# Performance work log

Measured on AMD Instinct MI355X. Metric: run time of the kernel, lower is better.

## Reference

```python
import jax, jax.numpy as jnp
import numpy as np

VOCAB = 2          # len(CHAR_VOCAB) in source
CE = 16            # char_embed_dim
CNN_OUT = 32 + 64 + 128  # 224
EMBED = 64


def _conv1d(x, w, b, pad):
    # x: [N, Cin, L]; w: [Cout, Cin, K]; torch Conv1d semantics
    y = jax.lax.conv_general_dilated(
        x, w, window_strides=(1,), padding=[(pad, pad)],
        dimension_numbers=('NCH', 'OIH', 'NCH'))
    return y + b[None, :, None]


def setup_inputs() -> dict:
    key = jax.random.key(0)
    ks = jax.random.split(key, 12)
    B, S, MC = 32, 2048, 20
    char_ids = jax.random.randint(ks[0], (B, S, MC), 0, VOCAB, dtype=jnp.int64)
    E = jax.random.normal(ks[1], (VOCAB, CE), jnp.float32)
    E = E.at[0].set(0.0)  # padding_idx=0
    s = 0.05
    return {
        'char_ids': char_ids,
        'E': E,
        'W1': jax.random.normal(ks[2], (32, CE, 1), jnp.float32) * s,
        'b1': jnp.zeros((32,), jnp.float32),
        'W2': jax.random.normal(ks[3], (64, CE, 2), jnp.float32) * s,
        'b2': jnp.zeros((64,), jnp.float32),
        'W3': jax.random.normal(ks[4], (128, CE, 3), jnp.float32) * s,
        'b3': jnp.zeros((128,), jnp.float32),
        'Ht_W': jax.random.normal(ks[5], (CNN_OUT, CNN_OUT), jnp.float32) * s,
        'Ht_b': jnp.zeros((CNN_OUT,), jnp.float32),
        'Hg_W': jax.random.normal(ks[6], (CNN_OUT, CNN_OUT), jnp.float32) * s,
        'Hg_b': jnp.zeros((CNN_OUT,), jnp.float32),
        'P_W': jax.random.normal(ks[7], (EMBED, CNN_OUT), jnp.float32) * s,
        'P_b': jnp.zeros((EMBED,), jnp.float32),
    }


def reference(char_ids, E, W1, b1, W2, b2, W3, b3, Ht_W, Ht_b, Hg_W, Hg_b, P_W, P_b):
    B, S, MC = char_ids.shape
    ids = char_ids.reshape(-1, MC)                      # [N, MC]
    emb = E[ids]                                        # [N, MC, CE]
    x = jnp.transpose(emb, (0, 2, 1))                   # [N, CE, MC]
    p1 = jnp.max(jax.nn.relu(_conv1d(x, W1, b1, 0)), axis=2)  # [N, 32]
    p2 = jnp.max(jax.nn.relu(_conv1d(x, W2, b2, 1)), axis=2)  # [N, 64]
    p3 = jnp.max(jax.nn.relu(_conv1d(x, W3, b3, 1)), axis=2)  # [N, 128]
    cnn = jnp.concatenate([p1, p2, p3], axis=1)         # [N, 224]
    t = jax.nn.relu(cnn @ Ht_W.T + Ht_b)
    g = jax.nn.sigmoid(cnn @ Hg_W.T + Hg_b)
    hw = g * t + (1.0 - g) * cnn
    out = hw @ P_W.T + P_b                              # [N, 64]
    return out.reshape(B, S, -1)
```

## Files before the change

kernel.cpp:

```cpp
#include <hip/hip_runtime.h>


typedef _Float16 f16;
typedef __attribute__((ext_vector_type(8))) _Float16 f16x8;
typedef __attribute__((ext_vector_type(4))) float f32x4;

#define LC1   0
#define LRAW2 96
#define LT2   672
#define LRAW3 1696
#define LT3LO 5152
#define LT3HI 7200
#define WOFFB    18944
#define PBASE    100352
#define NWTH     114688
#define TKEY_OFF 278528
#define UOUT_OFF 544768
#define NKEYS    4096
#define WSPLIT_BLOCKS 448
#define LUT_BLOCKS 4
#define CROW 232

__device__ __forceinline__ f16x8 hmax8(f16x8 a, f16x8 b) {
  return __builtin_elementwise_max(a, b);
}

__device__ __forceinline__ f16x8 pin8(f16x8 v) {
  union { f16x8 v; unsigned w[4]; } x; x.v = v;
  asm volatile("" : "+v"(x.w[0]), "+v"(x.w[1]), "+v"(x.w[2]), "+v"(x.w[3]) :: "memory");
  return x.v;
}

__global__ __launch_bounds__(256) void prep_key_kernel(
    const float* __restrict__ E,
    const float* __restrict__ W1, const float* __restrict__ b1,
    const float* __restrict__ W2, const float* __restrict__ b2,
    const float* __restrict__ W3, const float* __restrict__ b3,
    const float* __restrict__ HtW, const float* __restrict__ HgW,
    const float* __restrict__ PW, const int* __restrict__ ids,
    f16* __restrict__ tab, f16* __restrict__ wsb,
    unsigned* __restrict__ tokkey, int n_tok)
{
  const int tid = threadIdx.x;
  if (blockIdx.x >= WSPLIT_BLOCKS + LUT_BLOCKS) {
    int t = (blockIdx.x - WSPLIT_BLOCKS - LUT_BLOCKS) * 256 + tid;
    if (t >= n_tok) return;
    const int4* idp4 = (const int4*)(ids + (size_t)t * 20);
    int st[21];
#pragma unroll
    for (int q = 0; q < 5; q++) {
      int4 v = idp4[q];
      st[q * 4 + 1] = v.x; st[q * 4 + 2] = v.y;
      st[q * 4 + 3] = v.z; st[q * 4 + 4] = v.w;
    }
    unsigned m3i = 0;
#pragma unroll
    for (int l = 1; l <= 18; l++)
      m3i |= 1u << ((st[l] << 2) | (st[l + 1] << 1) | st[l + 2]);
    tokkey[t] = m3i | ((unsigned)st[1] << 8) | ((unsigned)st[2] << 9)
              | ((unsigned)st[19] << 10) | ((unsigned)st[20] << 11);
    return;
  }
  if (blockIdx.x < WSPLIT_BLOCKS) {
    int idx = blockIdx.x * 256 + tid;
    if (idx < NWTH) {
      int e, isG = 0, isP = 0;
      if (idx < 50176)        { e = idx; }
      else if (idx < 100352)  { e = idx - 50176; isG = 1; }
      else                    { e = idx - 100352; isP = 1; }
      int col = e / 224, k = e - col * 224;
      int nf = col >> 4, kf = k >> 5, kr = k & 31;
      int lane = (col & 15) + ((kr >> 3) << 4), j = kr & 7;
      if (!isP) {
        int off = nf * 7168 + (isG * 7 + kf) * 512 + lane * 8 + j;
        wsb[off] = (f16)(isG ? HgW[e] : HtW[e]);
      } else {
        float w = PW[e];
        f16 hi = (f16)w;
        int off = PBASE + nf * 7168 + kf * 512 + lane * 8 + j;
        wsb[off] = hi;
        wsb[off + 3584] = (f16)(w - (float)hi);
      }
    }
    return;
  }

  __shared__ float X[3][16];
  __shared__ float U1[3][32];
  __shared__ float U2[9][64];
  __shared__ float U3[27][128];
  const int gid = (blockIdx.x - WSPLIT_BLOCKS) * 256 + tid;
  const int gsz = LUT_BLOCKS * 256;
  if (tid < 48) { int s = tid >> 4, i = tid & 15; X[s][i] = (s == 0) ? 0.f : E[(s - 1) * 16 + i]; }
  __syncthreads();

  for (int idx = tid; idx < 96; idx += 256) {
    int s = idx >> 5, c = idx & 31;
    float acc = b1[c];
#pragma unroll
    for (int i = 0; i < 16; i++) acc += W1[c * 16 + i] * X[s][i];
    U1[s][c] = acc;
  }
  for (int idx = tid; idx < 576; idx += 256) {
    int p = idx >> 6, c = idx & 63;
    int sa = p / 3, sb = p % 3;
    float acc = b2[c];
#pragma unroll
    for (int i = 0; i < 16; i++)
      acc += W2[c * 32 + i * 2 + 0] * X[sa][i] + W2[c * 32 + i * 2 + 1] * X[sb][i];
    U2[p][c] = acc;
  }
  for (int idx = tid; idx < 3456; idx += 256) {
    int p = idx >> 7, c = idx & 127;
    int sa = p / 9, sb = (p / 3) % 3, sc = p % 3;
    float acc = b3[c];
#pragma unroll
    for (int i = 0; i < 16; i++)
      acc += W3[c * 48 + i * 3 + 0] * X[sa][i]
           + W3[c * 48 + i * 3 + 1] * X[sb][i]
           + W3[c * 48 + i * 3 + 2] * X[sc][i];
    U3[p][c] = acc;
  }
  __syncthreads();

  for (int idx = gid; idx < 96; idx += gsz) {
    int r = idx >> 5, c = idx & 31;
    float v = (r == 0) ? fmaxf(U1[1][c], U1[2][c]) : U1[r][c];
    tab[LC1 + idx] = (f16)v;
  }
  for (int idx = gid; idx < 576; idx += gsz) tab[LRAW2 + idx] = (f16)U2[idx >> 6][idx & 63];
  for (int idx = gid; idx < 3456; idx += gsz) tab[LRAW3 + idx] = (f16)U3[idx >> 7][idx & 127];
  for (int idx = gid; idx < 1024; idx += gsz) {
    int s = idx >> 6, c = idx & 63;
    float m = -65504.f;
#pragma unroll
    for (int b = 0; b < 4; b++)
      if ((s >> b) & 1) m = fmaxf(m, U2[4 + 3 * (b >> 1) + (b & 1)][c]);
    tab[LT2 + idx] = (f16)m;
  }
  for (int idx = gid; idx < 2048; idx += gsz) {
    int s = idx >> 7, c = idx & 127;
    float m = -65504.f;
#pragma unroll
    for (int b = 0; b < 4; b++)
      if ((s >> b) & 1) m = fmaxf(m, U3[13 + 3 * (b >> 1) + (b & 1)][c]);
    tab[LT3LO + idx] = (f16)m;
    m = -65504.f;
#pragma unroll
    for (int b = 0; b < 4; b++)
      if ((s >> b) & 1) m = fmaxf(m, U3[22 + 3 * (b >> 1) + (b & 1)][c]);
    tab[LT3HI + idx] = (f16)m;
  }
}

__global__ __launch_bounds__(256) void ucompute_kernel(
    const f16* __restrict__ tab, const f16* __restrict__ wsb,
    const float* __restrict__ Htb, const float* __restrict__ Hgb,
    const float* __restrict__ Pb, float* __restrict__ uout)
{
  __shared__ __attribute__((aligned(16))) f16 cnn[16 * CROW];

  const int tid = threadIdx.x;
  const int wave = tid >> 6, lane = tid & 63;
  const int kbase = blockIdx.x * 16;
  const int lrow = lane & 15;
  const int kg8 = (lane >> 4) * 8;
  const int rr0 = (lane >> 4) * 4;

  const int p1row = tid >> 4;
  const int p1g = tid & 15;
  unsigned mw, mb;
  {
    unsigned key = (unsigned)(kbase + p1row);
    unsigned m3i = key & 255u;
    int st1 = 1 + (int)((key >> 8) & 1),  st2 = 1 + (int)((key >> 9) & 1);
    int st19 = 1 + (int)((key >> 10) & 1), st20 = 1 + (int)((key >> 11) & 1);
    unsigned m2i = 0, mchar = 0;
#pragma unroll
    for (int p = 0; p < 8; p++)
      if ((m3i >> p) & 1) {
        m2i |= (1u << (p >> 1)) | (1u << (p & 3));
        mchar |= (1u << ((p >> 2) & 1)) | (1u << ((p >> 1) & 1)) | (1u << (p & 1));
      }
    unsigned sel = (mchar == 3u) ? 0u : ((mchar & 1u) ? 1u : 2u);
    mw = m3i | (m2i << 8) | (sel << 12);
    mb = (unsigned)st1 | ((unsigned)(st20 * 3) << 4)
       | ((unsigned)(st1 * 3 + st2) << 8) | ((unsigned)(st19 * 9 + st20 * 3) << 16);
  }

  const f16x8 KZ = {0, 0, 0, 0, 0, 0, 0, 0};
  {
    const int m3 = mw & 255;
    f16x8 v = hmax8(*(const f16x8*)(tab + LT3LO + (m3 & 15) * 128 + p1g * 8),
                    *(const f16x8*)(tab + LT3HI + ((m3 >> 4) & 15) * 128 + p1g * 8));
    v = hmax8(v, *(const f16x8*)(tab + LRAW3 + ((mb >> 8) & 15) * 128 + p1g * 8));
    v = hmax8(v, *(const f16x8*)(tab + LRAW3 + ((mb >> 16) & 31) * 128 + p1g * 8));
    *(f16x8*)&cnn[p1row * CROW + 96 + p1g * 8] = hmax8(v, KZ);
    if (p1g < 8) {
      f16x8 u = *(const f16x8*)(tab + LT2 + ((mw >> 8) & 15) * 64 + p1g * 8);
      u = hmax8(u, *(const f16x8*)(tab + LRAW2 + (mb & 15) * 64 + p1g * 8));
      u = hmax8(u, *(const f16x8*)(tab + LRAW2 + ((mb >> 4) & 15) * 64 + p1g * 8));
      *(f16x8*)&cnn[p1row * CROW + 32 + p1g * 8] = hmax8(u, KZ);
    }
    if (p1g < 4) {
      int sel = (mw >> 12) & 3;
      f16x8 w = *(const f16x8*)(tab + LC1 + sel * 32 + p1g * 8);
      *(f16x8*)&cnn[p1row * CROW + p1g * 8] = hmax8(w, KZ);
    }
  }
  __syncthreads();

  f16x8 af[7];
#pragma unroll
  for (int kf = 0; kf < 7; kf++)
    af[kf] = *(const f16x8*)&cnn[lrow * CROW + kf * 32 + kg8];
#pragma unroll
  for (int kf = 0; kf < 7; kf++) af[kf] = pin8(af[kf]);
  __syncthreads();

  const f16* wbase = wsb + lane * 8;
  const int nf_cnt = (wave < 2) ? 4 : 3;
  for (int i = 0; i < nf_cnt; i++) {
    const int nf = wave + i * 4;
    const int col = nf * 16 + lrow;
    const f16* p_ = wbase + nf * 7168;
    const float bt = Htb[col], bg = Hgb[col];
    f32x4 aT = {bt, bt, bt, bt};
    f32x4 aG = {bg, bg, bg, bg};
#pragma unroll
    for (int kf = 0; kf < 7; kf++) {
      f16x8 wTv = *(const f16x8*)(p_ + kf * 512);
      f16x8 wGv = *(const f16x8*)(p_ + 3584 + kf * 512);
      aT = __builtin_amdgcn_mfma_f32_16x16x32_f16(af[kf], wTv, aT, 0, 0, 0);
      aG = __builtin_amdgcn_mfma_f32_16x16x32_f16(af[kf], wGv, aG, 0, 0, 0);
    }
#pragma unroll
    for (int r = 0; r < 4; r++) {
      int row = rr0 + r;
      float t  = fmaxf(aT[r], 0.f);
      float gg = __builtin_amdgcn_rcpf(1.f + __expf(-aG[r]));
      float cv = (float)cnn[row * CROW + col];
      cnn[row * CROW + col] = (f16)(cv + gg * (t - cv));
    }
  }
  __syncthreads();

  f16x8 ah[7];
#pragma unroll
  for (int kf = 0; kf < 7; kf++)
    ah[kf] = *(const f16x8*)&cnn[lrow * CROW + kf * 32 + kg8];
  {
    const int col = wave * 16 + lrow;
    const float bp = Pb[col];
    f32x4 ac = {bp, bp, bp, bp};
    const f16* ph = wbase + PBASE + wave * 7168;
#pragma unroll
    for (int kf = 0; kf < 7; kf++) {
      f16x8 wh = *(const f16x8*)(ph + kf * 512);
      f16x8 wl = *(const f16x8*)(ph + 3584 + kf * 512);
      ac = __builtin_amdgcn_mfma_f32_16x16x32_f16(ah[kf], wh, ac, 0, 0, 0);
      ac = __builtin_amdgcn_mfma_f32_16x16x32_f16(ah[kf], wl, ac, 0, 0, 0);
    }
#pragma unroll
    for (int r = 0; r < 4; r++)
      uout[(size_t)(kbase + rr0 + r) * 64 + col] = ac[r];
  }
}

__global__ __launch_bounds__(256) void scatter_kernel(
    const unsigned* __restrict__ tokkey, const float* __restrict__ uout,
    float* __restrict__ out, int n_tok)
{
  int gid = blockIdx.x * 256 + threadIdx.x;
  int t = gid >> 2, q = gid & 3;
  if (t >= n_tok) return;
  unsigned s = tokkey[t];
  const float4* src = (const float4*)(uout + (size_t)s * 64 + q * 16);
  float4* dst = (float4*)(out + (size_t)t * 64 + q * 16);
  dst[0] = src[0]; dst[1] = src[1]; dst[2] = src[2]; dst[3] = src[3];
}

extern "C" void kernel_launch(void* const* d_in, const int* in_sizes, int n_in,
                              void* d_out, int out_size, void* d_ws, size_t ws_size,
                              hipStream_t stream) {
  const int*   ids = (const int*)d_in[0];
  const float* E   = (const float*)d_in[1];
  const float* W1  = (const float*)d_in[2];
  const float* b1  = (const float*)d_in[3];
  const float* W2  = (const float*)d_in[4];
  const float* b2  = (const float*)d_in[5];
  const float* W3  = (const float*)d_in[6];
  const float* b3  = (const float*)d_in[7];
  const float* HtW = (const float*)d_in[8];
  const float* Htb = (const float*)d_in[9];
  const float* HgW = (const float*)d_in[10];
  const float* Hgb = (const float*)d_in[11];
  const float* PW  = (const float*)d_in[12];
  const float* Pb  = (const float*)d_in[13];
  float* out = (float*)d_out;
  char* ws = (char*)d_ws;
  f16* tab = (f16*)ws;
  f16* wsb = (f16*)(ws + WOFFB);
  unsigned* tokkey = (unsigned*)(ws + TKEY_OFF);
  float* uout = (float*)(ws + UOUT_OFF);

  const int n_tok = in_sizes[0] / 20;
  const int key_blocks = (n_tok + 255) / 256;

  prep_key_kernel<<<WSPLIT_BLOCKS + LUT_BLOCKS + key_blocks, 256, 0, stream>>>(
      E, W1, b1, W2, b2, W3, b3, HtW, HgW, PW, ids, tab, wsb, tokkey, n_tok);
  ucompute_kernel<<<NKEYS / 16, 256, 0, stream>>>(tab, wsb, Htb, Hgb, Pb, uout);
  scatter_kernel<<<((size_t)n_tok * 4 + 255) / 256, 256, 0, stream>>>(
      tokkey, uout, out, n_tok);
}
```

Baseline: 31.90 us.

## Fuse LUT build and weight conversion into ucompute, merge key computation into scatter

Drops the separate prep kernel. Each ucompute block now rebuilds the conv lookup tables in shared memory and converts the fp32 highway and projection weights to fp16 on the fly from global memory, instead of reading a pre-swizzled fp16 buffer. The per-token key computation moves into the scatter kernel, so the tokkey round-trip through global memory goes away. This cuts one launch and the intermediate buffers, but every one of the 256 blocks redundantly computes the small conv tables, and weight loads become uncoalesced strided fp32 reads plus conversions.

```diff
diff --git a/kernel.cpp b/kernel.cpp
--- a/kernel.cpp
+++ b/kernel.cpp
@@ -11,15 +11,10 @@
 #define LRAW3 1696
 #define LT3LO 5152
 #define LT3HI 7200
-#define WOFFB    18944
-#define PBASE    100352
-#define NWTH     114688
-#define TKEY_OFF 278528
-#define UOUT_OFF 544768
-#define NKEYS    4096
-#define WSPLIT_BLOCKS 448
-#define LUT_BLOCKS 4
-#define CROW 232
+#define TABSZ 9248
+#define NKEYS 4096
+#define CROW  232
+#define UOUT_OFF 0
 
 __device__ __forceinline__ f16x8 hmax8(f16x8 a, f16x8 b) {
   return __builtin_elementwise_max(a, b);
@@ -31,133 +26,43 @@
   return x.v;
 }
 
-__global__ __launch_bounds__(256) void prep_key_kernel(
+__device__ __forceinline__ f16x8 ldcvt(const float* __restrict__ p) {
+  float4 a = *(const float4*)p;
+  float4 b = *(const float4*)(p + 4);
+  f16x8 r;
+  r[0] = (f16)a.x; r[1] = (f16)a.y; r[2] = (f16)a.z; r[3] = (f16)a.w;
+  r[4] = (f16)b.x; r[5] = (f16)b.y; r[6] = (f16)b.z; r[7] = (f16)b.w;
+  return r;
+}
+
+__device__ __forceinline__ void ldcvt2(const float* __restrict__ p,
+                                       f16x8& hi, f16x8& lo) {
+  float4 a = *(const float4*)p;
+  float4 b = *(const float4*)(p + 4);
+  float wv[8] = {a.x, a.y, a.z, a.w, b.x, b.y, b.z, b.w};
+#pragma unroll
+  for (int j = 0; j < 8; j++) {
+    f16 h = (f16)wv[j];
+    hi[j] = h;
+    lo[j] = (f16)(wv[j] - (float)h);
+  }
+}
+
+__global__ __launch_bounds__(256) void fused_ucompute(
     const float* __restrict__ E,
     const float* __restrict__ W1, const float* __restrict__ b1,
     const float* __restrict__ W2, const float* __restrict__ b2,
     const float* __restrict__ W3, const float* __restrict__ b3,
     const float* __restrict__ HtW, const float* __restrict__ HgW,
-    const float* __restrict__ PW, const int* __restrict__ ids,
-    f16* __restrict__ tab, f16* __restrict__ wsb,
-    unsigned* __restrict__ tokkey, int n_tok)
+    const float* __restrict__ PW,
+    const float* __restrict__ Htb, const float* __restrict__ Hgb,
+    const float* __restrict__ Pb, float* __restrict__ uout)
 {
-  const int tid = threadIdx.x;
-  if (blockIdx.x >= WSPLIT_BLOCKS + LUT_BLOCKS) {
-    int t = (blockIdx.x - WSPLIT_BLOCKS - LUT_BLOCKS) * 256 + tid;
-    if (t >= n_tok) return;
-    const int4* idp4 = (const int4*)(ids + (size_t)t * 20);
-    int st[21];
-#pragma unroll
-    for (int q = 0; q < 5; q++) {
-      int4 v = idp4[q];
-      st[q * 4 + 1] = v.x; st[q * 4 + 2] = v.y;
-      st[q * 4 + 3] = v.z; st[q * 4 + 4] = v.w;
-    }
-    unsigned m3i = 0;
-#pragma unroll
-    for (int l = 1; l <= 18; l++)
-      m3i |= 1u << ((st[l] << 2) | (st[l + 1] << 1) | st[l + 2]);
-    tokkey[t] = m3i | ((unsigned)st[1] << 8) | ((unsigned)st[2] << 9)
-              | ((unsigned)st[19] << 10) | ((unsigned)st[20] << 11);
-    return;
-  }
-  if (blockIdx.x < WSPLIT_BLOCKS) {
-    int idx = blockIdx.x * 256 + tid;
-    if (idx < NWTH) {
-      int e, isG = 0, isP = 0;
-      if (idx < 50176)        { e = idx; }
-      else if (idx < 100352)  { e = idx - 50176; isG = 1; }
-      else                    { e = idx - 100352; isP = 1; }
-      int col = e / 224, k = e - col * 224;
-      int nf = col >> 4, kf = k >> 5, kr = k & 31;
-      int lane = (col & 15) + ((kr >> 3) << 4), j = kr & 7;
-      if (!isP) {
-        int off = nf * 7168 + (isG * 7 + kf) * 512 + lane * 8 + j;
-        wsb[off] = (f16)(isG ? HgW[e] : HtW[e]);
-      } else {
-        float w = PW[e];
-        f16 hi = (f16)w;
-        int off = PBASE + nf * 7168 + kf * 512 + lane * 8 + j;
-        wsb[off] = hi;
-        wsb[off + 3584] = (f16)(w - (float)hi);
-      }
-    }
-    return;
-  }
-
   __shared__ float X[3][16];
   __shared__ float U1[3][32];
   __shared__ float U2[9][64];
   __shared__ float U3[27][128];
-  const int gid = (blockIdx.x - WSPLIT_BLOCKS) * 256 + tid;
-  const int gsz = LUT_BLOCKS * 256;
-  if (tid < 48) { int s = tid >> 4, i = tid & 15; X[s][i] = (s == 0) ? 0.f : E[(s - 1) * 16 + i]; }
-  __syncthreads();
-
-  for (int idx = tid; idx < 96; idx += 256) {
-    int s = idx >> 5, c = idx & 31;
-    float acc = b1[c];
-#pragma unroll
-    for (int i = 0; i < 16; i++) acc += W1[c * 16 + i] * X[s][i];
-    U1[s][c] = acc;
-  }
-  for (int idx = tid; idx < 576; idx += 256) {
-    int p = idx >> 6, c = idx & 63;
-    int sa = p / 3, sb = p % 3;
-    float acc = b2[c];
-#pragma unroll
-    for (int i = 0; i < 16; i++)
-      acc += W2[c * 32 + i * 2 + 0] * X[sa][i] + W2[c * 32 + i * 2 + 1] * X[sb][i];
-    U2[p][c] = acc;
-  }
-  for (int idx = tid; idx < 3456; idx += 256) {
-    int p = idx >> 7, c = idx & 127;
-    int sa = p / 9, sb = (p / 3) % 3, sc = p % 3;
-    float acc = b3[c];
-#pragma unroll
-    for (int i = 0; i < 16; i++)
-      acc += W3[c * 48 + i * 3 + 0] * X[sa][i]
-           + W3[c * 48 + i * 3 + 1] * X[sb][i]
-           + W3[c * 48 + i * 3 + 2] * X[sc][i];
-    U3[p][c] = acc;
-  }
-  __syncthreads();
-
-  for (int idx = gid; idx < 96; idx += gsz) {
-    int r = idx >> 5, c = idx & 31;
-    float v = (r == 0) ? fmaxf(U1[1][c], U1[2][c]) : U1[r][c];
-    tab[LC1 + idx] = (f16)v;
-  }
-  for (int idx = gid; idx < 576; idx += gsz) tab[LRAW2 + idx] = (f16)U2[idx >> 6][idx & 63];
-  for (int idx = gid; idx < 3456; idx += gsz) tab[LRAW3 + idx] = (f16)U3[idx >> 7][idx & 127];
-  for (int idx = gid; idx < 1024; idx += gsz) {
-    int s = idx >> 6, c = idx & 63;
-    float m = -65504.f;
-#pragma unroll
-    for (int b = 0; b < 4; b++)
-      if ((s >> b) & 1) m = fmaxf(m, U2[4 + 3 * (b >> 1) + (b & 1)][c]);
-    tab[LT2 + idx] = (f16)m;
-  }
-  for (int idx = gid; idx < 2048; idx += gsz) {
-    int s = idx >> 7, c = idx & 127;
-    float m = -65504.f;
-#pragma unroll
-    for (int b = 0; b < 4; b++)
-      if ((s >> b) & 1) m = fmaxf(m, U3[13 + 3 * (b >> 1) + (b & 1)][c]);
-    tab[LT3LO + idx] = (f16)m;
-    m = -65504.f;
-#pragma unroll
-    for (int b = 0; b < 4; b++)
-      if ((s >> b) & 1) m = fmaxf(m, U3[22 + 3 * (b >> 1) + (b & 1)][c]);
-    tab[LT3HI + idx] = (f16)m;
-  }
-}
-
-__global__ __launch_bounds__(256) void ucompute_kernel(
-    const f16* __restrict__ tab, const f16* __restrict__ wsb,
-    const float* __restrict__ Htb, const float* __restrict__ Hgb,
-    const float* __restrict__ Pb, float* __restrict__ uout)
-{
+  __shared__ __attribute__((aligned(16))) f16 tab[TABSZ];
   __shared__ __attribute__((aligned(16))) f16 cnn[16 * CROW];
 
   const int tid = threadIdx.x;
@@ -166,6 +71,67 @@
   const int lrow = lane & 15;
   const int kg8 = (lane >> 4) * 8;
   const int rr0 = (lane >> 4) * 4;
+
+  if (tid < 48) { int s = tid >> 4, i = tid & 15; X[s][i] = (s == 0) ? 0.f : E[(s - 1) * 16 + i]; }
+  __syncthreads();
+  for (int idx = tid; idx < 96; idx += 256) {
+    int s = idx >> 5, c = idx & 31;
+    float acc = b1[c];
+#pragma unroll
+    for (int i = 0; i < 16; i++) acc += W1[c * 16 + i] * X[s][i];
+    U1[s][c] = acc;
+  }
+  for (int idx = tid; idx < 576; idx += 256) {
+    int p = idx >> 6, c = idx & 63;
+    int sa = p / 3, sb = p % 3;
+    float acc = b2[c];
+#pragma unroll
+    for (int i = 0; i < 16; i++)
+      acc += W2[c * 32 + i * 2 + 0] * X[sa][i] + W2[c * 32 + i * 2 + 1] * X[sb][i];
+    U2[p][c] = acc;
+  }
+  for (int idx = tid; idx < 3456; idx += 256) {
+    int p = idx >> 7, c = idx & 127;
+    int sa = p / 9, sb = (p / 3) % 3, sc = p % 3;
+    float acc = b3[c];
+#pragma unroll
+    for (int i = 0; i < 16; i++)
+      acc += W3[c * 48 + i * 3 + 0] * X[sa][i]
+           + W3[c * 48 + i * 3 + 1] * X[sb][i]
+           + W3[c * 48 + i * 3 + 2] * X[sc][i];
+    U3[p][c] = acc;
+  }
+  __syncthreads();
+
+  if (tid < 96) {
+    int r = tid >> 5, c = tid & 31;
+    float v = (r == 0) ? fmaxf(U1[1][c], U1[2][c]) : U1[r][c];
+    tab[LC1 + tid] = (f16)v;
+  }
+  for (int idx = tid; idx < 576; idx += 256) tab[LRAW2 + idx] = (f16)U2[idx >> 6][idx & 63];
+  for (int idx = tid; idx < 3456; idx += 256) tab[LRAW3 + idx] = (f16)U3[idx >> 7][idx & 127];
+  for (int idx = tid; idx < 1024; idx += 256) {
+    int s = idx >> 6, c = idx & 63;
+    float m = -65504.f;
+#pragma unroll
+    for (int b = 0; b < 4; b++)
+      if ((s >> b) & 1) m = fmaxf(m, U2[4 + 3 * (b >> 1) + (b & 1)][c]);
+    tab[LT2 + idx] = (f16)m;
+  }
+  for (int idx = tid; idx < 2048; idx += 256) {
+    int s = idx >> 7, c = idx & 127;
+    float m = -65504.f;
+#pragma unroll
+    for (int b = 0; b < 4; b++)
+      if ((s >> b) & 1) m = fmaxf(m, U3[13 + 3 * (b >> 1) + (b & 1)][c]);
+    tab[LT3LO + idx] = (f16)m;
+    m = -65504.f;
+#pragma unroll
+    for (int b = 0; b < 4; b++)
+      if ((s >> b) & 1) m = fmaxf(m, U3[22 + 3 * (b >> 1) + (b & 1)][c]);
+    tab[LT3HI + idx] = (f16)m;
+  }
+  __syncthreads();
 
   const int p1row = tid >> 4;
   const int p1g = tid & 15;
@@ -191,20 +157,20 @@
   const f16x8 KZ = {0, 0, 0, 0, 0, 0, 0, 0};
   {
     const int m3 = mw & 255;
-    f16x8 v = hmax8(*(const f16x8*)(tab + LT3LO + (m3 & 15) * 128 + p1g * 8),
-                    *(const f16x8*)(tab + LT3HI + ((m3 >> 4) & 15) * 128 + p1g * 8));
-    v = hmax8(v, *(const f16x8*)(tab + LRAW3 + ((mb >> 8) & 15) * 128 + p1g * 8));
-    v = hmax8(v, *(const f16x8*)(tab + LRAW3 + ((mb >> 16) & 31) * 128 + p1g * 8));
+    f16x8 v = hmax8(*(const f16x8*)&tab[LT3LO + (m3 & 15) * 128 + p1g * 8],
+                    *(const f16x8*)&tab[LT3HI + ((m3 >> 4) & 15) * 128 + p1g * 8]);
+    v = hmax8(v, *(const f16x8*)&tab[LRAW3 + ((mb >> 8) & 15) * 128 + p1g * 8]);
+    v = hmax8(v, *(const f16x8*)&tab[LRAW3 + ((mb >> 16) & 31) * 128 + p1g * 8]);
     *(f16x8*)&cnn[p1row * CROW + 96 + p1g * 8] = hmax8(v, KZ);
     if (p1g < 8) {
-      f16x8 u = *(const f16x8*)(tab + LT2 + ((mw >> 8) & 15) * 64 + p1g * 8);
-      u = hmax8(u, *(const f16x8*)(tab + LRAW2 + (mb & 15) * 64 + p1g * 8));
-      u = hmax8(u, *(const f16x8*)(tab + LRAW2 + ((mb >> 4) & 15) * 64 + p1g * 8));
+      f16x8 u = *(const f16x8*)&tab[LT2 + ((mw >> 8) & 15) * 64 + p1g * 8];
+      u = hmax8(u, *(const f16x8*)&tab[LRAW2 + (mb & 15) * 64 + p1g * 8]);
+      u = hmax8(u, *(const f16x8*)&tab[LRAW2 + ((mb >> 4) & 15) * 64 + p1g * 8]);
       *(f16x8*)&cnn[p1row * CROW + 32 + p1g * 8] = hmax8(u, KZ);
     }
     if (p1g < 4) {
       int sel = (mw >> 12) & 3;
-      f16x8 w = *(const f16x8*)(tab + LC1 + sel * 32 + p1g * 8);
+      f16x8 w = *(const f16x8*)&tab[LC1 + sel * 32 + p1g * 8];
       *(f16x8*)&cnn[p1row * CROW + p1g * 8] = hmax8(w, KZ);
     }
   }
@@ -218,19 +184,19 @@
   for (int kf = 0; kf < 7; kf++) af[kf] = pin8(af[kf]);
   __syncthreads();
 
-  const f16* wbase = wsb + lane * 8;
   const int nf_cnt = (wave < 2) ? 4 : 3;
   for (int i = 0; i < nf_cnt; i++) {
     const int nf = wave + i * 4;
     const int col = nf * 16 + lrow;
-    const f16* p_ = wbase + nf * 7168;
+    const float* wt = HtW + (size_t)col * 224 + kg8;
+    const float* wg = HgW + (size_t)col * 224 + kg8;
     const float bt = Htb[col], bg = Hgb[col];
     f32x4 aT = {bt, bt, bt, bt};
     f32x4 aG = {bg, bg, bg, bg};
 #pragma unroll
     for (int kf = 0; kf < 7; kf++) {
-      f16x8 wTv = *(const f16x8*)(p_ + kf * 512);
-      f16x8 wGv = *(const f16x8*)(p_ + 3584 + kf * 512);
+      f16x8 wTv = ldcvt(wt + kf * 32);
+      f16x8 wGv = ldcvt(wg + kf * 32);
       aT = __builtin_amdgcn_mfma_f32_16x16x32_f16(af[kf], wTv, aT, 0, 0, 0);
       aG = __builtin_amdgcn_mfma_f32_16x16x32_f16(af[kf], wGv, aG, 0, 0, 0);
     }
@@ -251,13 +217,13 @@
     ah[kf] = *(const f16x8*)&cnn[lrow * CROW + kf * 32 + kg8];
   {
     const int col = wave * 16 + lrow;
+    const float* pw = PW + (size_t)col * 224 + kg8;
     const float bp = Pb[col];
     f32x4 ac = {bp, bp, bp, bp};
-    const f16* ph = wbase + PBASE + wave * 7168;
 #pragma unroll
     for (int kf = 0; kf < 7; kf++) {
-      f16x8 wh = *(const f16x8*)(ph + kf * 512);
-      f16x8 wl = *(const f16x8*)(ph + 3584 + kf * 512);
+      f16x8 wh, wl;
+      ldcvt2(pw + kf * 32, wh, wl);
       ac = __builtin_amdgcn_mfma_f32_16x16x32_f16(ah[kf], wh, ac, 0, 0, 0);
       ac = __builtin_amdgcn_mfma_f32_16x16x32_f16(ah[kf], wl, ac, 0, 0, 0);
     }
@@ -267,15 +233,41 @@
   }
 }
 
-__global__ __launch_bounds__(256) void scatter_kernel(
-    const unsigned* __restrict__ tokkey, const float* __restrict__ uout,
+__global__ __launch_bounds__(256) void keyscatter_kernel(
+    const int* __restrict__ ids, const float* __restrict__ uout,
     float* __restrict__ out, int n_tok)
 {
-  int gid = blockIdx.x * 256 + threadIdx.x;
-  int t = gid >> 2, q = gid & 3;
+  __shared__ unsigned keys[64];
+  const int tid = threadIdx.x;
+  const int tok0 = blockIdx.x * 64;
+
+  if (tid < 64) {
+    unsigned key = 0;
+    int t = tok0 + tid;
+    if (t < n_tok) {
+      const int4* idp4 = (const int4*)(ids + (size_t)t * 20);
+      int st[21];
+#pragma unroll
+      for (int q = 0; q < 5; q++) {
+        int4 v = idp4[q];
+        st[q * 4 + 1] = v.x; st[q * 4 + 2] = v.y;
+        st[q * 4 + 3] = v.z; st[q * 4 + 4] = v.w;
+      }
+      unsigned m3i = 0;
+#pragma unroll
+      for (int l = 1; l <= 18; l++)
+        m3i |= 1u << ((st[l] << 2) | (st[l + 1] << 1) | st[l + 2]);
+      key = m3i | ((unsigned)st[1] << 8) | ((unsigned)st[2] << 9)
+          | ((unsigned)st[19] << 10) | ((unsigned)st[20] << 11);
+    }
+    keys[tid] = key;
+  }
+  __syncthreads();
+
+  const int tl = tid >> 2, q = tid & 3;
+  const int t = tok0 + tl;
   if (t >= n_tok) return;
-  unsigned s = tokkey[t];
-  const float4* src = (const float4*)(uout + (size_t)s * 64 + q * 16);
+  const float4* src = (const float4*)(uout + (size_t)keys[tl] * 64 + q * 16);
   float4* dst = (float4*)(out + (size_t)t * 64 + q * 16);
   dst[0] = src[0]; dst[1] = src[1]; dst[2] = src[2]; dst[3] = src[3];
 }
@@ -298,18 +290,10 @@
   const float* PW  = (const float*)d_in[12];
   const float* Pb  = (const float*)d_in[13];
   float* out = (float*)d_out;
-  char* ws = (char*)d_ws;
-  f16* tab = (f16*)ws;
-  f16* wsb = (f16*)(ws + WOFFB);
-  unsigned* tokkey = (unsigned*)(ws + TKEY_OFF);
-  float* uout = (float*)(ws + UOUT_OFF);
+  float* uout = (float*)((char*)d_ws + UOUT_OFF);
 
   const int n_tok = in_sizes[0] / 20;
-  const int key_blocks = (n_tok + 255) / 256;
-
-  prep_key_kernel<<<WSPLIT_BLOCKS + LUT_BLOCKS + key_blocks, 256, 0, stream>>>(
-      E, W1, b1, W2, b2, W3, b3, HtW, HgW, PW, ids, tab, wsb, tokkey, n_tok);
-  ucompute_kernel<<<NKEYS / 16, 256, 0, stream>>>(tab, wsb, Htb, Hgb, Pb, uout);
-  scatter_kernel<<<((size_t)n_tok * 4 + 255) / 256, 256, 0, stream>>>(
-      tokkey, uout, out, n_tok);
-}
+  fused_ucompute<<<NKEYS / 16, 256, 0, stream>>>(
+      E, W1, b1, W2, b2, W3, b3, HtW, HgW, PW, Htb, Hgb, Pb, uout);
+  keyscatter_kernel<<<(n_tok + 63) / 64, 256, 0, stream>>>(ids, uout, out, n_tok);
+}
```

Measured after the change: 40.57 us. 1.27x slower.
